# Kernel tuning notes

Hardware: AMD Instinct MI355X
Metric: run time of the kernel (lower is better)

## Reference

```python
import jax, jax.numpy as jnp
import numpy as np

DIM = 1024
HEAD_DIM = 64
NUM_HEADS = DIM // HEAD_DIM
SCALE = HEAD_DIM ** -0.5


def setup_inputs() -> dict:
    key = jax.random.key(0)
    ks = jax.random.split(key, 12)
    b, n = 4, 2048
    std = DIM ** -0.5
    inp = {
        'words': jax.random.normal(ks[0], (b, n, DIM), jnp.float32),
        'position': jax.random.normal(ks[1], (b, n, DIM), jnp.float32),
        'conscious': jax.random.normal(ks[2], (b, n, DIM), jnp.float32),
        # projection weights stored as [in, out] (torch Linear W^T)
        'w_wq': jax.random.normal(ks[3], (DIM, DIM), jnp.float32) * std,
        'w_wk': jax.random.normal(ks[4], (DIM, DIM), jnp.float32) * std,
        'w_wv': jax.random.normal(ks[5], (DIM, DIM), jnp.float32) * std,
        'w_pq': jax.random.normal(ks[6], (DIM, DIM), jnp.float32) * std,
        'w_pk': jax.random.normal(ks[7], (DIM, DIM), jnp.float32) * std,
        'w_cq': jax.random.normal(ks[8], (DIM, DIM), jnp.float32) * std,
        'w_ck': jax.random.normal(ks[9], (DIM, DIM), jnp.float32) * std,
        'w_out': jax.random.normal(ks[10], (DIM, DIM), jnp.float32) * std,
        'b_out': jax.random.normal(ks[11], (DIM,), jnp.float32) * 0.01,
    }
    return inp


def _heads(x):
    b, n, _ = x.shape
    return x.reshape(b, n, NUM_HEADS, HEAD_DIM).transpose(0, 2, 1, 3)  # b h n d


def reference(words, position, conscious, w_wq, w_wk, w_wv, w_pq, w_pk, w_cq, w_ck, w_out, b_out):
    # fused multi-source q/k: sum of three projections per source
    q = _heads(words @ w_wq + position @ w_pq + conscious @ w_cq)
    k = _heads(words @ w_wk + position @ w_pk + conscious @ w_ck)
    v = _heads(words @ w_wv)
    sim = jnp.einsum('bhid,bhjd->bhij', q, k) * SCALE
    attn = jax.nn.softmax(sim, axis=-1)
    out = jnp.einsum('bhij,bhjd->bhid', attn, v)
    b, h, n, d = out.shape
    out = out.transpose(0, 2, 1, 3).reshape(b, n, h * d)
    return out @ w_out + b_out
```

## Files before the change

kernel.cpp:

```cpp
#include <hip/hip_runtime.h>
#include <hip/hip_bf16.h>

typedef __bf16 bf16_t;
typedef __attribute__((ext_vector_type(8))) __bf16 bf16x8;
typedef __attribute__((ext_vector_type(4))) float f32x4;
typedef __attribute__((ext_vector_type(16))) float f32x16;

__device__ __forceinline__ void gld_lds16(const void* g, void* l) {
  __builtin_amdgcn_global_load_lds((const __attribute__((address_space(1))) void*)g,
                                   (__attribute__((address_space(3))) void*)l, 16, 0, 0);
}

__global__ __launch_bounds__(256) void cast_concat(
    const float* __restrict__ w, const float* __restrict__ p,
    const float* __restrict__ c, bf16_t* __restrict__ X)
{
  unsigned idx = blockIdx.x * 256u + threadIdx.x;
  unsigned src = idx >> 21;
  unsigned rem = idx & ((1u << 21) - 1);
  unsigned row = rem >> 8;
  unsigned k4  = (rem & 255u) * 4u;
  const float* s = (src == 0) ? w : (src == 1) ? p : c;
  f32x4 v = *(const f32x4*)(s + (size_t)row * 1024 + k4);
  ushort4 u;
  u.x = __builtin_bit_cast(unsigned short, (bf16_t)v[0]);
  u.y = __builtin_bit_cast(unsigned short, (bf16_t)v[1]);
  u.z = __builtin_bit_cast(unsigned short, (bf16_t)v[2]);
  u.w = __builtin_bit_cast(unsigned short, (bf16_t)v[3]);
  *(ushort4*)(X + (size_t)row * 3072 + src * 1024 + k4) = u;
}

__global__ __launch_bounds__(256) void transpose_all(
    const float* __restrict__ w_wq, const float* __restrict__ w_pq,
    const float* __restrict__ w_cq, const float* __restrict__ w_wk,
    const float* __restrict__ w_pk, const float* __restrict__ w_ck,
    const float* __restrict__ w_wv, const float* __restrict__ w_out,
    bf16_t* __restrict__ Wqkt, bf16_t* __restrict__ Wvt, bf16_t* __restrict__ Wot)
{
  __shared__ float t[32][33];
  const int z = blockIdx.z;
  const float* src; bf16_t* dst; int dstride, koff, roff;
  switch (z) {
    case 0: src = w_wq;  dst = Wqkt; dstride = 3072; koff = 0;    roff = 0;    break;
    case 1: src = w_pq;  dst = Wqkt; dstride = 3072; koff = 1024; roff = 0;    break;
    case 2: src = w_cq;  dst = Wqkt; dstride = 3072; koff = 2048; roff = 0;    break;
    case 3: src = w_wk;  dst = Wqkt; dstride = 3072; koff = 0;    roff = 1024; break;
    case 4: src = w_pk;  dst = Wqkt; dstride = 3072; koff = 1024; roff = 1024; break;
    case 5: src = w_ck;  dst = Wqkt; dstride = 3072; koff = 2048; roff = 1024; break;
    case 6: src = w_wv;  dst = Wvt;  dstride = 1024; koff = 0;    roff = 0;    break;
    default: src = w_out; dst = Wot; dstride = 1024; koff = 0;    roff = 0;    break;
  }
  int bx = blockIdx.x, by = blockIdx.y;
  int x = bx * 32 + threadIdx.x;
  int y0 = by * 32;
  for (int i = threadIdx.y; i < 32; i += 8)
    t[i][threadIdx.x] = src[(size_t)(y0 + i) * 1024 + x];
  __syncthreads();
  int n0 = bx * 32;
  for (int i = threadIdx.y; i < 32; i += 8)
    dst[(size_t)(n0 + i + roff) * dstride + koff + y0 + threadIdx.x] =
        (bf16_t)t[threadIdx.x][i];
}

template<int EPI>
__global__ __launch_bounds__(256, 2) void gemm_bt(
    const bf16_t* __restrict__ A, int lda,
    const bf16_t* __restrict__ Bt, int K,
    void* __restrict__ Cout, void* __restrict__ Cout2,
    const float* __restrict__ bias, float scale)
{
  __shared__ bf16_t As[128 * 32];
  __shared__ bf16_t Bs[128 * 32];
  const int tid  = threadIdx.x;
  const int wave = tid >> 6, lane = tid & 63;
  const int m0 = blockIdx.y * 128, n0 = blockIdx.x * 128;
  const int wr = (wave >> 1) * 64, wc = (wave & 1) * 64;
  const int lrow = lane & 15, lch = lane >> 4;

  f32x4 acc[4][4] = {};

  for (int k0 = 0; k0 < K; k0 += 32) {
    __syncthreads();
#pragma unroll
    for (int t = 0; t < 2; ++t) {
      int cc = t * 256 + tid;
      int row = cc >> 2, pp = cc & 3;
      int kswz = (pp ^ (row & 3)) * 8;
      gld_lds16(A  + (size_t)(m0 + row) * lda + k0 + kswz, &As[cc * 8]);
      gld_lds16(Bt + (size_t)(n0 + row) * K   + k0 + kswz, &Bs[cc * 8]);
    }
    __syncthreads();
    bf16x8 a[4], b[4];
#pragma unroll
    for (int i = 0; i < 4; ++i) {
      int r = wr + i * 16 + lrow;
      a[i] = *(const bf16x8*)&As[r * 32 + ((lch ^ (r & 3)) * 8)];
    }
#pragma unroll
    for (int i = 0; i < 4; ++i) {
      int r = wc + i * 16 + lrow;
      b[i] = *(const bf16x8*)&Bs[r * 32 + ((lch ^ (r & 3)) * 8)];
    }
#pragma unroll
    for (int i = 0; i < 4; ++i)
#pragma unroll
      for (int j = 0; j < 4; ++j)
        acc[i][j] = __builtin_amdgcn_mfma_f32_16x16x32_bf16(a[i], b[j], acc[i][j], 0, 0, 0);
  }

  const int g = lane >> 4, cl = lane & 15;
  if (EPI == 0) {
    bf16_t* Qo = (bf16_t*)Cout;
    bf16_t* Ko = (bf16_t*)Cout2;
#pragma unroll
    for (int i = 0; i < 4; ++i) {
      int m_base = m0 + wr + i * 16 + g * 4;
      int bb = m_base >> 11, nn = m_base & 2047;
#pragma unroll
      for (int j = 0; j < 4; ++j) {
        int col = n0 + wc + j * 16 + cl;
        bf16_t* dst = (col < 1024) ? Qo : Ko;
        int cc2 = col & 1023;
        float sc = (col < 1024) ? scale : 1.0f;
        int h = cc2 >> 6, d = cc2 & 63;
        size_t base = ((size_t)(bb * 16 + h) * 2048 + nn) * 64 + d;
#pragma unroll
        for (int r = 0; r < 4; ++r)
          dst[base + (size_t)r * 64] = (bf16_t)(acc[i][j][r] * sc);
      }
    }
  } else if (EPI == 1) {
    bf16_t* Vo = (bf16_t*)Cout;
#pragma unroll
    for (int i = 0; i < 4; ++i) {
      int m_base = m0 + wr + i * 16 + g * 4;
      int bb = m_base >> 11, nn = m_base & 2047;
#pragma unroll
      for (int j = 0; j < 4; ++j) {
        int col = n0 + wc + j * 16 + cl;
        int h = col >> 6, d = col & 63;
        ushort4 u;
        u.x = __builtin_bit_cast(unsigned short, (bf16_t)acc[i][j][0]);
        u.y = __builtin_bit_cast(unsigned short, (bf16_t)acc[i][j][1]);
        u.z = __builtin_bit_cast(unsigned short, (bf16_t)acc[i][j][2]);
        u.w = __builtin_bit_cast(unsigned short, (bf16_t)acc[i][j][3]);
        *(ushort4*)(Vo + ((size_t)(bb * 16 + h) * 64 + d) * 2048 + nn) = u;
      }
    }
  } else {
    float* Co = (float*)Cout;
#pragma unroll
    for (int i = 0; i < 4; ++i) {
      int m_base = m0 + wr + i * 16 + g * 4;
#pragma unroll
      for (int j = 0; j < 4; ++j) {
        int col = n0 + wc + j * 16 + cl;
        float bv = bias[col];
#pragma unroll
        for (int r = 0; r < 4; ++r)
          Co[(size_t)(m_base + r) * 1024 + col] = acc[i][j][r] + bv;
      }
    }
  }
}

__global__ __launch_bounds__(512, 2) void attn_kernel(
    const bf16_t* __restrict__ Q, const bf16_t* __restrict__ Kb,
    const bf16_t* __restrict__ Vt, bf16_t* __restrict__ O)
{
  __shared__ bf16_t Ks[2][64 * 64];
  __shared__ bf16_t Vs[2][64 * 64];

  const int fid = blockIdx.x;
  const int swz = (fid & 7) * 64 + (fid >> 3);
  const int bh = swz >> 3, qt = swz & 7;
  const int bb = bh >> 4, h = bh & 15;

  const int tid = threadIdx.x, wave = tid >> 6, lane = tid & 63;
  const int lq = lane & 31;
  const int lh = lane >> 5;

  const bf16_t* Qb    = Q  + ((size_t)bh * 2048 + qt * 256) * 64;
  const bf16_t* Kbase = Kb + (size_t)bh * 2048 * 64;
  const bf16_t* Vbase = Vt + (size_t)bh * 64 * 2048;

  auto STAGE = [&](int buf, int kv0) {
    int row = tid >> 3, pp = tid & 7;
    int sgr = (pp ^ (row & 7)) * 8;
    gld_lds16(Kbase + (size_t)(kv0 + row) * 64 + sgr, &Ks[buf][tid * 8]);
    gld_lds16(Vbase + (size_t)row * 2048 + kv0 + sgr, &Vs[buf][tid * 8]);
  };

  STAGE(0, 0);

  bf16x8 qf[4];
#pragma unroll
  for (int kf = 0; kf < 4; ++kf)
    qf[kf] = *(const bf16x8*)(Qb + (size_t)(wave * 32 + lq) * 64 + kf * 16 + lh * 8);

  f32x16 acc[2] = {};
  float m_run = -1.0e30f, l_run = 0.f;

  for (int t = 0; t < 32; ++t) {
    const int buf = t & 1;
    if (t < 31) {
      STAGE(buf ^ 1, (t + 1) * 64);
      asm volatile("s_waitcnt vmcnt(2)" ::: "memory");
    } else {
      asm volatile("s_waitcnt vmcnt(0)" ::: "memory");
    }
    __builtin_amdgcn_s_barrier();
    asm volatile("" ::: "memory");

    f32x16 st[2] = {};
#pragma unroll
    for (int nb = 0; nb < 2; ++nb) {
      int r = nb * 32 + lq;
#pragma unroll
      for (int kf = 0; kf < 4; ++kf) {
        bf16x8 ka = *(const bf16x8*)&Ks[buf][r * 64 + (((kf * 2 + lh) ^ (r & 7)) * 8)];
        st[nb] = __builtin_amdgcn_mfma_f32_32x32x16_bf16(ka, qf[kf], st[nb], 0, 0, 0);
      }
    }

    float tmax = st[0][0];
#pragma unroll
    for (int nb = 0; nb < 2; ++nb)
#pragma unroll
      for (int rg = 0; rg < 16; ++rg)
        tmax = fmaxf(tmax, st[nb][rg]);
    tmax = fmaxf(tmax, __shfl_xor(tmax, 32));

    if (!__all(tmax <= m_run + 8.0f)) {
      float mnew = fmaxf(m_run, tmax);
      float corr = __builtin_amdgcn_exp2f(m_run - mnew);
      m_run = mnew;
      l_run *= corr;
#pragma unroll
      for (int db = 0; db < 2; ++db)
#pragma unroll
        for (int rg = 0; rg < 16; ++rg)
          acc[db][rg] *= corr;
    }

    float sm = 0.f;
#pragma unroll
    for (int nb = 0; nb < 2; ++nb)
#pragma unroll
      for (int rg = 0; rg < 16; ++rg) {
        float p = __builtin_amdgcn_exp2f(st[nb][rg] - m_run);
        st[nb][rg] = p;
        sm += p;
      }
    sm += __shfl_xor(sm, 32);
    l_run += sm;

#pragma unroll
    for (int ks = 0; ks < 4; ++ks) {
      const int nb = ks >> 1;
      const int R = (ks & 1) * 8;
      unsigned x0, x1, y0, y1;
      asm("v_cvt_pk_bf16_f32 %0, %1, %2" : "=v"(x0) : "v"(st[nb][R + 0]), "v"(st[nb][R + 1]));
      asm("v_cvt_pk_bf16_f32 %0, %1, %2" : "=v"(x1) : "v"(st[nb][R + 2]), "v"(st[nb][R + 3]));
      asm("v_cvt_pk_bf16_f32 %0, %1, %2" : "=v"(y0) : "v"(st[nb][R + 4]), "v"(st[nb][R + 5]));
      asm("v_cvt_pk_bf16_f32 %0, %1, %2" : "=v"(y1) : "v"(st[nb][R + 6]), "v"(st[nb][R + 7]));
      asm volatile("v_permlane32_swap_b32 %0, %1" : "+v"(x0), "+v"(y0));
      asm volatile("v_permlane32_swap_b32 %0, %1" : "+v"(x1), "+v"(y1));
      int4 pw;
      pw.x = (int)x0; pw.y = (int)x1; pw.z = (int)y0; pw.w = (int)y1;
      bf16x8 pb = __builtin_bit_cast(bf16x8, pw);
#pragma unroll
      for (int db = 0; db < 2; ++db) {
        int r = db * 32 + lq;
        bf16x8 va = *(const bf16x8*)&Vs[buf][r * 64 + (((ks * 2 + lh) ^ (r & 7)) * 8)];
        acc[db] = __builtin_amdgcn_mfma_f32_32x32x16_bf16(va, pb, acc[db], 0, 0, 0);
      }
    }

    asm volatile("s_waitcnt lgkmcnt(0)" ::: "memory");
    __builtin_amdgcn_s_barrier();
    asm volatile("" ::: "memory");
  }

  float inv = 1.0f / l_run;
  int nn = qt * 256 + wave * 32 + lq;
  size_t obase = ((size_t)bb * 2048 + nn) * 1024 + h * 64;
#pragma unroll
  for (int db = 0; db < 2; ++db)
#pragma unroll
    for (int rr = 0; rr < 4; ++rr) {
      ushort4 u;
      u.x = __builtin_bit_cast(unsigned short, (bf16_t)(acc[db][rr * 4 + 0] * inv));
      u.y = __builtin_bit_cast(unsigned short, (bf16_t)(acc[db][rr * 4 + 1] * inv));
      u.z = __builtin_bit_cast(unsigned short, (bf16_t)(acc[db][rr * 4 + 2] * inv));
      u.w = __builtin_bit_cast(unsigned short, (bf16_t)(acc[db][rr * 4 + 3] * inv));
      *(ushort4*)(O + obase + db * 32 + rr * 8 + lh * 4) = u;
    }
}

extern "C" void kernel_launch(void* const* d_in, const int* in_sizes, int n_in,
                              void* d_out, int out_size, void* d_ws, size_t ws_size,
                              hipStream_t stream) {
  const float* words     = (const float*)d_in[0];
  const float* position  = (const float*)d_in[1];
  const float* conscious = (const float*)d_in[2];
  const float* w_wq  = (const float*)d_in[3];
  const float* w_wk  = (const float*)d_in[4];
  const float* w_wv  = (const float*)d_in[5];
  const float* w_pq  = (const float*)d_in[6];
  const float* w_pk  = (const float*)d_in[7];
  const float* w_cq  = (const float*)d_in[8];
  const float* w_ck  = (const float*)d_in[9];
  const float* w_out = (const float*)d_in[10];
  const float* b_out = (const float*)d_in[11];

  char* ws = (char*)d_ws;
  bf16_t* Xcat = (bf16_t*)(ws);
  bf16_t* Wqkt = (bf16_t*)(ws + 50331648);
  bf16_t* Wvt  = (bf16_t*)(ws + 62914560);
  bf16_t* Wot  = (bf16_t*)(ws + 65011712);
  bf16_t* Qb   = (bf16_t*)(ws + 67108864);
  bf16_t* Kbf  = (bf16_t*)(ws + 83886080);
  bf16_t* Vtb  = (bf16_t*)(ws + 100663296);
  bf16_t* Ob   = (bf16_t*)(ws + 117440512);

  cast_concat<<<24576, 256, 0, stream>>>(words, position, conscious, Xcat);

  transpose_all<<<dim3(32, 32, 8), dim3(32, 8), 0, stream>>>(
      w_wq, w_pq, w_cq, w_wk, w_pk, w_ck, w_wv, w_out, Wqkt, Wvt, Wot);

  gemm_bt<0><<<dim3(16, 64), 256, 0, stream>>>(Xcat, 3072, Wqkt, 3072, Qb, Kbf,
                                               nullptr, 0.125f * 1.44269504f);
  gemm_bt<1><<<dim3(8, 64), 256, 0, stream>>>(Xcat, 3072, Wvt, 1024, Vtb, nullptr,
                                              nullptr, 1.0f);

  attn_kernel<<<512, 512, 0, stream>>>(Qb, Kbf, Vtb, Ob);

  gemm_bt<2><<<dim3(8, 64), 256, 0, stream>>>(Ob, 1024, Wot, 1024, (float*)d_out, nullptr,
                                              b_out, 1.0f);
}
```

Baseline: 330.6 us.

## Replace QK projection GEMM with 256x256 double-buffered tiled kernel

Adds a dedicated QK projection GEMM that uses 256x256 output tiles with 512 threads, BK=64, and two LDS buffers filled by direct global-to-LDS loads. Loads are overlapped with MFMA work using explicit vmcnt waits, and the MFMA section runs at raised wave priority. An XCD-aware block swizzle is meant to improve L2 reuse. The larger tiles cut global and LDS traffic per FLOP for the largest GEMM (8192x2048x3072), but 256 blocks on 256 CUs leaves a single wave of work with more registers per thread.

```diff
diff --git a/kernel.cpp b/kernel.cpp
--- a/kernel.cpp
+++ b/kernel.cpp
@@ -62,12 +62,109 @@
         (bf16_t)t[threadIdx.x][i];
 }
 
+__global__ __launch_bounds__(512, 2) void gemm256_qk(
+    const bf16_t* __restrict__ A, int lda,
+    const bf16_t* __restrict__ Bt, int K,
+    bf16_t* __restrict__ Qo, bf16_t* __restrict__ Ko, float scale, int nbx)
+{
+  __shared__ bf16_t As[2][256 * 64];
+  __shared__ bf16_t Bs[2][256 * 64];
+
+  const int tid = threadIdx.x;
+  const int wave = tid >> 6, lane = tid & 63;
+  const int wm = wave >> 2, wn = wave & 3;
+  const int lrow = lane & 15, lch = lane >> 4;
+
+  const int nwg = gridDim.x, cpx = nwg >> 3;
+  const int id  = blockIdx.x;
+  const int swz = (id & 7) * cpx + (id >> 3);
+  const int mb = swz / nbx, nb = swz % nbx;
+  const int m0 = mb * 256, n0 = nb * 256;
+
+  const int srow = tid >> 3, spp = tid & 7;
+
+  auto STAGE = [&](int buf, int k0) {
+#pragma unroll
+    for (int i = 0; i < 4; ++i) {
+      int r = i * 64 + srow;
+      int gsw = (spp ^ (r & 7)) * 8;
+      gld_lds16(A + (size_t)(m0 + r) * lda + k0 + gsw, &As[buf][r * 64 + spp * 8]);
+    }
+#pragma unroll
+    for (int i = 0; i < 4; ++i) {
+      int r = i * 64 + srow;
+      int gsw = (spp ^ (r & 7)) * 8;
+      gld_lds16(Bt + (size_t)(n0 + r) * K + k0 + gsw, &Bs[buf][r * 64 + spp * 8]);
+    }
+  };
+
+  const int NT = K >> 6;
+  STAGE(0, 0);
+  STAGE(1, 64);
+
+  f32x4 acc[8][4] = {};
+
+  for (int kt = 0; kt < NT; ++kt) {
+    const int cur = kt & 1;
+    if (kt < NT - 1) {
+      asm volatile("s_waitcnt vmcnt(8)" ::: "memory");
+    } else {
+      asm volatile("s_waitcnt vmcnt(0)" ::: "memory");
+    }
+    asm volatile("s_barrier" ::: "memory");
+
+#pragma unroll
+    for (int ks = 0; ks < 2; ++ks) {
+      bf16x8 af[8], bfr[4];
+#pragma unroll
+      for (int m = 0; m < 8; ++m) {
+        int r = wm * 128 + m * 16 + lrow;
+        af[m] = *(const bf16x8*)&As[cur][r * 64 + (((ks * 4 + lch) ^ (r & 7)) * 8)];
+      }
+#pragma unroll
+      for (int n = 0; n < 4; ++n) {
+        int r = wn * 64 + n * 16 + lrow;
+        bfr[n] = *(const bf16x8*)&Bs[cur][r * 64 + (((ks * 4 + lch) ^ (r & 7)) * 8)];
+      }
+      __builtin_amdgcn_s_setprio(1);
+#pragma unroll
+      for (int m = 0; m < 8; ++m)
+#pragma unroll
+        for (int n = 0; n < 4; ++n)
+          acc[m][n] = __builtin_amdgcn_mfma_f32_16x16x32_bf16(af[m], bfr[n], acc[m][n], 0, 0, 0);
+      __builtin_amdgcn_s_setprio(0);
+    }
+
+    asm volatile("s_waitcnt lgkmcnt(0)" ::: "memory");
+    asm volatile("s_barrier" ::: "memory");
+    if (kt + 2 < NT) STAGE(cur, (kt + 2) * 64);
+  }
+
+  const int g = lane >> 4, cl = lane & 15;
+#pragma unroll
+  for (int m = 0; m < 8; ++m) {
+    int m_base = m0 + wm * 128 + m * 16 + g * 4;
+    int bb = m_base >> 11, nn = m_base & 2047;
+#pragma unroll
+    for (int n = 0; n < 4; ++n) {
+      int col = n0 + wn * 64 + n * 16 + cl;
+      bf16_t* dst = (col < 1024) ? Qo : Ko;
+      int cc2 = col & 1023;
+      float sc = (col < 1024) ? scale : 1.0f;
+      int h = cc2 >> 6, d = cc2 & 63;
+      size_t base = ((size_t)(bb * 16 + h) * 2048 + nn) * 64 + d;
+#pragma unroll
+      for (int r = 0; r < 4; ++r)
+        dst[base + (size_t)r * 64] = (bf16_t)(acc[m][n][r] * sc);
+    }
+  }
+}
+
 template<int EPI>
 __global__ __launch_bounds__(256, 2) void gemm_bt(
     const bf16_t* __restrict__ A, int lda,
     const bf16_t* __restrict__ Bt, int K,
-    void* __restrict__ Cout, void* __restrict__ Cout2,
-    const float* __restrict__ bias, float scale)
+    void* __restrict__ Cout, const float* __restrict__ bias, float scale)
 {
   __shared__ bf16_t As[128 * 32];
   __shared__ bf16_t Bs[128 * 32];
@@ -109,27 +206,7 @@
   }
 
   const int g = lane >> 4, cl = lane & 15;
-  if (EPI == 0) {
-    bf16_t* Qo = (bf16_t*)Cout;
-    bf16_t* Ko = (bf16_t*)Cout2;
-#pragma unroll
-    for (int i = 0; i < 4; ++i) {
-      int m_base = m0 + wr + i * 16 + g * 4;
-      int bb = m_base >> 11, nn = m_base & 2047;
-#pragma unroll
-      for (int j = 0; j < 4; ++j) {
-        int col = n0 + wc + j * 16 + cl;
-        bf16_t* dst = (col < 1024) ? Qo : Ko;
-        int cc2 = col & 1023;
-        float sc = (col < 1024) ? scale : 1.0f;
-        int h = cc2 >> 6, d = cc2 & 63;
-        size_t base = ((size_t)(bb * 16 + h) * 2048 + nn) * 64 + d;
-#pragma unroll
-        for (int r = 0; r < 4; ++r)
-          dst[base + (size_t)r * 64] = (bf16_t)(acc[i][j][r] * sc);
-      }
-    }
-  } else if (EPI == 1) {
+  if (EPI == 1) {
     bf16_t* Vo = (bf16_t*)Cout;
 #pragma unroll
     for (int i = 0; i < 4; ++i) {
@@ -329,13 +406,12 @@
   transpose_all<<<dim3(32, 32, 8), dim3(32, 8), 0, stream>>>(
       w_wq, w_pq, w_cq, w_wk, w_pk, w_ck, w_wv, w_out, Wqkt, Wvt, Wot);
 
-  gemm_bt<0><<<dim3(16, 64), 256, 0, stream>>>(Xcat, 3072, Wqkt, 3072, Qb, Kbf,
-                                               nullptr, 0.125f * 1.44269504f);
-  gemm_bt<1><<<dim3(8, 64), 256, 0, stream>>>(Xcat, 3072, Wvt, 1024, Vtb, nullptr,
-                                              nullptr, 1.0f);
+  gemm256_qk<<<256, 512, 0, stream>>>(Xcat, 3072, Wqkt, 3072, Qb, Kbf,
+                                      0.125f * 1.44269504f, 8);
+  gemm_bt<1><<<dim3(8, 64), 256, 0, stream>>>(Xcat, 3072, Wvt, 1024, Vtb, nullptr, 1.0f);
 
   attn_kernel<<<512, 512, 0, stream>>>(Qb, Kbf, Vtb, Ob);
 
-  gemm_bt<2><<<dim3(8, 64), 256, 0, stream>>>(Ob, 1024, Wot, 1024, (float*)d_out, nullptr,
+  gemm_bt<2><<<dim3(8, 64), 256, 0, stream>>>(Ob, 1024, Wot, 1024, (float*)d_out,
                                               b_out, 1.0f);
 }
```

New measurement: 296.8 us. 1.11x faster.
